# Performance work log

Hardware: AMD Instinct MI355X
Metric: run time of the kernel (lower is better)

The kernel has to match this reference:

```python
import jax, jax.numpy as jnp
import numpy as np

EPS = 1e-8  # torch CosineSimilarity eps


def setup_inputs() -> dict:
    key = jax.random.key(0)
    ks = jax.random.split(key, 7)
    B, N, T, C, M, MEM, IN, E = 8, 512, 64, 128, 32, 20, 2, 4
    s = 0.05  # keep softmax logits in a sane range (xavier-like scale)
    return {
        "input": jax.random.normal(ks[0], (B, N, T, IN), jnp.float32),
        "hidden": jax.random.normal(ks[1], (E, B, N, T, C), jnp.float32),
        "memory": jax.random.normal(ks[2], (MEM, M), jnp.float32) * s,
        "input_query": jax.random.normal(ks[3], (IN, M), jnp.float32) * s,
        "Wq": jax.random.normal(ks[4], (E, C, M), jnp.float32) * s,
        "Wk": jax.random.normal(ks[5], (E, C, M), jnp.float32) * s,
        "Wv": jax.random.normal(ks[6], (E, C, M), jnp.float32) * s,
    }


def _cosine_sim(a, b):
    # torch.nn.CosineSimilarity(dim=-1): dot / (max(||a||,eps)*max(||b||,eps))
    num = jnp.sum(a * b, axis=-1)
    na = jnp.maximum(jnp.linalg.norm(a, axis=-1), EPS)
    nb = jnp.maximum(jnp.linalg.norm(b, axis=-1), EPS)
    return num / (na * nb)


def reference(input, hidden, memory, input_query, Wq, Wk, Wv):
    B, N, T, _ = input.shape
    out_dim = 1
    # query_mem: soft read from memory bank -> [B,N,T,mem_hid]
    q_in = jnp.einsum("bnti,im->bntm", input, input_query)
    mem_score = jax.nn.softmax(jnp.einsum("bntm,km->bntk", q_in, memory), axis=-1)
    memories = jnp.einsum("bntk,km->bntm", mem_score, memory)
    # per-expert self-attention over T (vectorized over the 4 experts)
    q = jnp.einsum("ebntc,ecm->ebntm", hidden, Wq)
    k = jnp.einsum("ebntc,ecm->ebntm", hidden, Wk)
    v = jnp.einsum("ebntc,ecm->ebntm", hidden, Wv)
    energy = jnp.einsum("ebntm,ebnsm->ebnts", q, k)  # [E,B,N,T,T]
    att = jnp.einsum("ebnts,ebnsm->ebntm", jax.nn.softmax(energy, axis=-1), v)
    # cosine similarity of memory read vs each expert's attended hidden
    scores = _cosine_sim(memories[None], att)  # [E,B,N,T]
    scores = jnp.moveaxis(scores, 0, -1)  # [B,N,T,E]
    out = jnp.broadcast_to(scores[..., None, :], (B, N, T, out_dim, scores.shape[-1]))
    return out
```

## Files before the change

kernel.cpp:

```cpp
#include <hip/hip_runtime.h>
#include <hip/hip_bf16.h>
#include <math.h>

#define Bc 8
#define Nc 512
#define Tc 64
#define Cc 128
#define Mc 32
#define MEMc 20
#define Ec 4

#define LDK  40
#define LDVT 72

typedef short bf16x8 __attribute__((ext_vector_type(8)));
typedef float f32x4  __attribute__((ext_vector_type(4)));

__device__ __forceinline__ unsigned short f2bfu(float f) {
    return __builtin_bit_cast(unsigned short, __float2bfloat16(f));
}
__device__ __forceinline__ unsigned pk2bf(float x, float y) {
    return ((unsigned)f2bfu(y) << 16) | (unsigned)f2bfu(x);
}

__device__ __forceinline__ void gload_lds16(const void* g, void* l) {
    __builtin_amdgcn_global_load_lds(
        (const __attribute__((address_space(1))) unsigned int*)g,
        (__attribute__((address_space(3))) unsigned int*)l, 16, 0, 0);
}

__global__ void prep(const float* __restrict__ Wq, const float* __restrict__ Wk,
                     const float* __restrict__ Wv, const float* __restrict__ membank,
                     const float* __restrict__ iq,
                     short* __restrict__ wt_img, short* __restrict__ bankM,
                     float* __restrict__ G2) {
    const int t = threadIdx.x;
    if (blockIdx.x < 192) {
        int idx = blockIdx.x * 256 + t;
        int e   = idx / 12288;
        int r   = idx - e * 12288;
        int mat = r >> 12;
        int m   = (r >> 7) & 31;
        int c   = r & 127;
        const float* W = (mat == 0) ? Wq : (mat == 1) ? Wk : Wv;
        const int dst = e * 12288 + mat * 4096 + m * 128 + (c ^ ((m & 7) << 3));
        wt_img[dst] = (short)f2bfu(W[((size_t)e * Cc + c) * Mc + m]);
    } else {
        for (int idx = t; idx < Mc * 32; idx += 256) {
            int m = idx >> 5, k = idx & 31;
            bankM[idx] = (short)f2bfu((k < MEMc) ? membank[k * Mc + m] : 0.f);
        }
        if (t < MEMc) {
            float g0 = 0.f, g1 = 0.f;
            for (int m = 0; m < Mc; ++m) {
                float b = membank[t * Mc + m];
                g0 = fmaf(iq[m], b, g0);
                g1 = fmaf(iq[Mc + m], b, g1);
            }
            G2[2 * t]     = g0;
            G2[2 * t + 1] = g1;
        }
    }
}

__device__ __forceinline__ void proj(const short* __restrict__ sh_wt, const bf16x8* a,
                                     int lo, int hi,
                                     f32x4 q_[2], f32x4 k_[2], f32x4 v_[2]) {
    #pragma unroll
    for (int nt = 0; nt < 2; ++nt)
        q_[nt] = k_[nt] = v_[nt] = (f32x4){0.f, 0.f, 0.f, 0.f};
    const int swz = (lo & 7) << 3;
    int col[4];
    #pragma unroll
    for (int kt = 0; kt < 4; ++kt) col[kt] = (kt * 32 + hi * 8) ^ swz;
    const short* wrow = sh_wt + lo * 128;
    #pragma unroll
    for (int nt = 0; nt < 2; ++nt) {
        const short* p0 = wrow + nt * 2048;
        #pragma unroll
        for (int kt = 0; kt < 4; ++kt) {
            const bf16x8 wq = *(const bf16x8*)(p0 + col[kt]);
            const bf16x8 wk = *(const bf16x8*)(p0 + 4096 + col[kt]);
            const bf16x8 wv = *(const bf16x8*)(p0 + 8192 + col[kt]);
            q_[nt] = __builtin_amdgcn_mfma_f32_16x16x32_bf16(wq, a[kt], q_[nt], 0, 0, 0);
            k_[nt] = __builtin_amdgcn_mfma_f32_16x16x32_bf16(wk, a[kt], k_[nt], 0, 0, 0);
            v_[nt] = __builtin_amdgcn_mfma_f32_16x16x32_bf16(wv, a[kt], v_[nt], 0, 0, 0);
        }
    }
}

__device__ __forceinline__ void gate_pd(const float* __restrict__ G2, float2 in2, unsigned pd[10]) {
    #pragma unroll
    for (int kp = 0; kp < 10; ++kp) {
        const float4 g = *(const float4*)(G2 + 4 * kp);
        pd[kp] = pk2bf(__expf(in2.x * g.x + in2.y * g.y),
                       __expf(in2.x * g.z + in2.y * g.w));
    }
}

__device__ __forceinline__ void mem_read(const short* __restrict__ bankM,
                                         const unsigned pd[10], int lo, int hi, int w,
                                         f32x4 am[2]) {
    am[0] = am[1] = (f32x4){0.f, 0.f, 0.f, 0.f};
    const int addrD = (w * 16 + lo) * 4;
    unsigned Wd[10];
    #pragma unroll
    for (int u = 0; u < 10; ++u)
        Wd[u] = __builtin_amdgcn_ds_bpermute(addrD, (int)pd[u]);
    unsigned b[4];
    #pragma unroll
    for (int u = 0; u < 4; ++u) {
        const unsigned l_ = (hi == 0) ? Wd[u] : Wd[4 + u];
        const unsigned h_ = (u < 2) ? ((hi == 2) ? Wd[8 + u] : 0u) : 0u;
        b[u] = (hi < 2) ? l_ : h_;
    }
    const bf16x8 bp2 = __builtin_bit_cast(bf16x8, (uint4){b[0], b[1], b[2], b[3]});
    #pragma unroll
    for (int nt = 0; nt < 2; ++nt) {
        const bf16x8 ab = *(const bf16x8*)(bankM + (nt * 16 + lo) * 32 + hi * 8);
        am[nt] = __builtin_amdgcn_mfma_f32_16x16x32_bf16(ab, bp2, am[nt], 0, 0, 0);
    }
}

__device__ __forceinline__ void attend_store(
    const short* __restrict__ shk, const short* __restrict__ shv,
    const unsigned q_pk[4], const f32x4 am[2],
    int lo, int hi, int w, int A01, int A23, int addrA, int addrB,
    int bn, int e, float* __restrict__ out) {
    unsigned pw[4][2];
    {
        unsigned l0 = __builtin_amdgcn_ds_bpermute(A01, (int)q_pk[0]);
        unsigned h0_ = __builtin_amdgcn_ds_bpermute(A01, (int)q_pk[2]);
        unsigned l1 = __builtin_amdgcn_ds_bpermute(A01, (int)q_pk[1]);
        unsigned h1_ = __builtin_amdgcn_ds_bpermute(A01, (int)q_pk[3]);
        unsigned l2 = __builtin_amdgcn_ds_bpermute(A23, (int)q_pk[0]);
        unsigned h2_ = __builtin_amdgcn_ds_bpermute(A23, (int)q_pk[2]);
        unsigned l3 = __builtin_amdgcn_ds_bpermute(A23, (int)q_pk[1]);
        unsigned h3_ = __builtin_amdgcn_ds_bpermute(A23, (int)q_pk[3]);
        const bf16x8 bq = __builtin_bit_cast(bf16x8, (uint4){
            (hi < 2) ? l0 : h0_, (hi < 2) ? l1 : h1_,
            (hi < 2) ? l2 : h2_, (hi < 2) ? l3 : h3_});
        #pragma unroll
        for (int st = 0; st < 4; ++st) {
            const bf16x8 akf = *(const bf16x8*)&shk[(st * 16 + lo) * LDK + hi * 8];
            const f32x4 en = __builtin_amdgcn_mfma_f32_16x16x32_bf16(
                akf, bq, (f32x4){0.f, 0.f, 0.f, 0.f}, 0, 0, 0);
            pw[st][0] = pk2bf(__expf(en[0]), __expf(en[1]));
            pw[st][1] = pk2bf(__expf(en[2]), __expf(en[3]));
        }
    }
    f32x4 av[2];
    av[0] = av[1] = (f32x4){0.f, 0.f, 0.f, 0.f};
    {
        bf16x8 bp[2];
        #pragma unroll
        for (int kt = 0; kt < 2; ++kt) {
            unsigned wrd[4];
            #pragma unroll
            for (int uu = 0; uu < 4; ++uu) {
                const int adr = (uu < 2) ? addrA : addrB;
                const unsigned ev = __builtin_amdgcn_ds_bpermute(adr, (int)pw[2 * kt][uu & 1]);
                const unsigned od = __builtin_amdgcn_ds_bpermute(adr, (int)pw[2 * kt + 1][uu & 1]);
                wrd[uu] = (hi < 2) ? ev : od;
            }
            bp[kt] = __builtin_bit_cast(bf16x8, (uint4){wrd[0], wrd[1], wrd[2], wrd[3]});
        }
        #pragma unroll
        for (int nt = 0; nt < 2; ++nt)
            #pragma unroll
            for (int kt = 0; kt < 2; ++kt) {
                const bf16x8 avt = *(const bf16x8*)&shv[(nt * 16 + lo) * LDVT + kt * 32 + hi * 8];
                av[nt] = __builtin_amdgcn_mfma_f32_16x16x32_bf16(avt, bp[kt], av[nt], 0, 0, 0);
            }
    }
    float d = 0.f, na = 0.f, nb = 0.f;
    #pragma unroll
    for (int nt = 0; nt < 2; ++nt)
        #pragma unroll
        for (int j = 0; j < 4; ++j) {
            const float av_ = av[nt][j], am_ = am[nt][j];
            d  = fmaf(av_, am_, d);
            na = fmaf(av_, av_, na);
            nb = fmaf(am_, am_, nb);
        }
    d  += __shfl_xor(d, 16);  d  += __shfl_xor(d, 32);
    na += __shfl_xor(na, 16); na += __shfl_xor(na, 32);
    nb += __shfl_xor(nb, 16); nb += __shfl_xor(nb, 32);
    if (hi == 0) {
        const float denom = fmaxf(sqrtf(na), 1e-8f) * fmaxf(sqrtf(nb), 1e-8f);
        out[((size_t)bn * Tc + w * 16 + lo) * Ec + e] = d / denom;
    }
}

__global__ __launch_bounds__(256, 4) void mg_mfma(
    const float* __restrict__ input,
    const float* __restrict__ hidden,
    const short* __restrict__ wt_img,
    const short* __restrict__ bankM,
    const float* __restrict__ G2,
    float* __restrict__ out)
{
    __shared__ __align__(16) short sh_wt[12288];
    __shared__ __align__(16) short sh_k [Tc * LDK];
    __shared__ __align__(16) short sh_vt[Mc * LDVT];

    const int t    = threadIdx.x;
    const int w    = t >> 6;
    const int lane = t & 63;
    const int lo   = lane & 15;
    const int hi   = lane >> 4;
    const int e    = blockIdx.x >> 11;
    const int bn0  = (blockIdx.x & 2047) * 2;
    const int bn1  = bn0 + 1;

    const int A01   = (((hi & 1) * 32) + lo) << 2;
    const int A23   = A01 + 64;
    const int addrA = (((hi & 1) * 2 + 0) * 16 + lo) * 4;
    const int addrB = (((hi & 1) * 2 + 1) * 16 + lo) * 4;

    {
        const short* gsrc = wt_img + (size_t)e * 12288 + w * 512 + lane * 8;
        short* ldst = sh_wt + w * 512;
        #pragma unroll
        for (int c = 0; c < 6; ++c)
            gload_lds16(gsrc + c * 2048, ldst + c * 2048);
    }

    const float2 in2_0 = *(const float2*)(input + ((size_t)bn0 * Tc + lane) * 2);
    const float2 in2_1 = *(const float2*)(input + ((size_t)bn1 * Tc + lane) * 2);
    float4 h[8];
    {
        const float* hr0 = hidden + (((size_t)(e * 4096 + bn0)) * Tc + w * 16 + lo) * Cc + hi * 8;
        #pragma unroll
        for (int kt = 0; kt < 4; ++kt) {
            h[2 * kt]     = *(const float4*)(hr0 + kt * 32);
            h[2 * kt + 1] = *(const float4*)(hr0 + kt * 32 + 4);
        }
    }

    f32x4 am0[2];
    {
        unsigned pd0[10];
        gate_pd(G2, in2_0, pd0);
        mem_read(bankM, pd0, lo, hi, w, am0);
    }

    bf16x8 a0[4];
    #pragma unroll
    for (int kt = 0; kt < 4; ++kt) {
        const float4 x = h[2 * kt], y = h[2 * kt + 1];
        a0[kt] = __builtin_bit_cast(bf16x8, (uint4){pk2bf(x.x, x.y), pk2bf(x.z, x.w),
                                                    pk2bf(y.x, y.y), pk2bf(y.z, y.w)});
    }

    __syncthreads();

    unsigned q_pk0[4];
    {
        f32x4 q_[2], k_[2], v_[2];
        proj(sh_wt, a0, lo, hi, q_, k_, v_);
        #pragma unroll
        for (int nt = 0; nt < 2; ++nt) {
            *(uint2*)&sh_k[(w * 16 + lo) * LDK + nt * 16 + hi * 4] =
                (uint2){pk2bf(k_[nt][0], k_[nt][1]), pk2bf(k_[nt][2], k_[nt][3])};
            #pragma unroll
            for (int j = 0; j < 4; ++j)
                sh_vt[(nt * 16 + hi * 4 + j) * LDVT + w * 16 + lo] = (short)f2bfu(v_[nt][j]);
            q_pk0[nt * 2]     = pk2bf(q_[nt][0], q_[nt][1]);
            q_pk0[nt * 2 + 1] = pk2bf(q_[nt][2], q_[nt][3]);
        }
    }

    __syncthreads();

    {
        const float* hr1 = hidden + (((size_t)(e * 4096 + bn1)) * Tc + w * 16 + lo) * Cc + hi * 8;
        #pragma unroll
        for (int kt = 0; kt < 4; ++kt) {
            h[2 * kt]     = *(const float4*)(hr1 + kt * 32);
            h[2 * kt + 1] = *(const float4*)(hr1 + kt * 32 + 4);
        }
    }

    f32x4 am1[2];
    {
        unsigned pd1[10];
        gate_pd(G2, in2_1, pd1);
        mem_read(bankM, pd1, lo, hi, w, am1);
    }

    attend_store(sh_k, sh_vt, q_pk0, am0, lo, hi, w, A01, A23, addrA, addrB, bn0, e, out);

    bf16x8 a1[4];
    #pragma unroll
    for (int kt = 0; kt < 4; ++kt) {
        const float4 x = h[2 * kt], y = h[2 * kt + 1];
        a1[kt] = __builtin_bit_cast(bf16x8, (uint4){pk2bf(x.x, x.y), pk2bf(x.z, x.w),
                                                    pk2bf(y.x, y.y), pk2bf(y.z, y.w)});
    }

    __syncthreads();

    unsigned q_pk1[4];
    {
        f32x4 q_[2], k_[2], v_[2];
        proj(sh_wt, a1, lo, hi, q_, k_, v_);
        #pragma unroll
        for (int nt = 0; nt < 2; ++nt) {
            *(uint2*)&sh_k[(w * 16 + lo) * LDK + nt * 16 + hi * 4] =
                (uint2){pk2bf(k_[nt][0], k_[nt][1]), pk2bf(k_[nt][2], k_[nt][3])};
            #pragma unroll
            for (int j = 0; j < 4; ++j)
                sh_vt[(nt * 16 + hi * 4 + j) * LDVT + w * 16 + lo] = (short)f2bfu(v_[nt][j]);
            q_pk1[nt * 2]     = pk2bf(q_[nt][0], q_[nt][1]);
            q_pk1[nt * 2 + 1] = pk2bf(q_[nt][2], q_[nt][3]);
        }
    }

    __syncthreads();

    attend_store(sh_k, sh_vt, q_pk1, am1, lo, hi, w, A01, A23, addrA, addrB, bn1, e, out);
}

extern "C" void kernel_launch(void* const* d_in, const int* in_sizes, int n_in,
                              void* d_out, int out_size, void* d_ws, size_t ws_size,
                              hipStream_t stream) {
    const float* input   = (const float*)d_in[0];
    const float* hidden  = (const float*)d_in[1];
    const float* membank = (const float*)d_in[2];
    const float* iq      = (const float*)d_in[3];
    const float* Wq      = (const float*)d_in[4];
    const float* Wk      = (const float*)d_in[5];
    const float* Wv      = (const float*)d_in[6];
    float* out = (float*)d_out;

    short* wt_img = (short*)d_ws;
    short* bankM  = (short*)((char*)d_ws + 98304);
    float* G2     = (float*)((char*)d_ws + 100352);

    prep<<<193, 256, 0, stream>>>(Wq, Wk, Wv, membank, iq, wt_img, bankM, G2);
    mg_mfma<<<Ec * Bc * Nc / 2, 256, 0, stream>>>(input, hidden, wt_img, bankM, G2, out);
}
```

Measured before the change: 121.4 us.

## Process eight (b,n) units per block with software-pipelined hidden loads

Each block now handles eight consecutive (b,n) units instead of two, so the weight image is staged into LDS once per eight units rather than once per two. The per-unit phase prefetches the next unit's hidden rows before doing the memory read and attention for the current unit, overlapping global loads with compute. The cost is four times fewer blocks (2048), which reduces parallelism and tail balance, plus more live registers from the eight preloaded input pairs.

```diff
diff --git a/kernel.cpp b/kernel.cpp
--- a/kernel.cpp
+++ b/kernel.cpp
@@ -12,6 +12,8 @@
 
 #define LDK  40
 #define LDVT 72
+
+#define UNITS 8
 
 typedef short bf16x8 __attribute__((ext_vector_type(8)));
 typedef float f32x4  __attribute__((ext_vector_type(4)));
@@ -63,9 +65,27 @@
     }
 }
 
-__device__ __forceinline__ void proj(const short* __restrict__ sh_wt, const bf16x8* a,
-                                     int lo, int hi,
-                                     f32x4 q_[2], f32x4 k_[2], f32x4 v_[2]) {
+__device__ __forceinline__ void load_hidden(const float* __restrict__ hrow, float4 h[8]) {
+    #pragma unroll
+    for (int kt = 0; kt < 4; ++kt) {
+        h[2 * kt]     = *(const float4*)(hrow + kt * 32);
+        h[2 * kt + 1] = *(const float4*)(hrow + kt * 32 + 4);
+    }
+}
+__device__ __forceinline__ void conv_a(const float4 h[8], bf16x8 a[4]) {
+    #pragma unroll
+    for (int kt = 0; kt < 4; ++kt) {
+        const float4 x = h[2 * kt], y = h[2 * kt + 1];
+        a[kt] = __builtin_bit_cast(bf16x8, (uint4){pk2bf(x.x, x.y), pk2bf(x.z, x.w),
+                                                   pk2bf(y.x, y.y), pk2bf(y.z, y.w)});
+    }
+}
+
+__device__ __forceinline__ void proj_store(const short* __restrict__ sh_wt, const bf16x8 a[4],
+                                           int lo, int hi, int w,
+                                           short* __restrict__ sh_k, short* __restrict__ sh_vt,
+                                           unsigned q_pk[4]) {
+    f32x4 q_[2], k_[2], v_[2];
     #pragma unroll
     for (int nt = 0; nt < 2; ++nt)
         q_[nt] = k_[nt] = v_[nt] = (f32x4){0.f, 0.f, 0.f, 0.f};
@@ -86,6 +106,16 @@
             k_[nt] = __builtin_amdgcn_mfma_f32_16x16x32_bf16(wk, a[kt], k_[nt], 0, 0, 0);
             v_[nt] = __builtin_amdgcn_mfma_f32_16x16x32_bf16(wv, a[kt], v_[nt], 0, 0, 0);
         }
+    }
+    #pragma unroll
+    for (int nt = 0; nt < 2; ++nt) {
+        *(uint2*)&sh_k[(w * 16 + lo) * LDK + nt * 16 + hi * 4] =
+            (uint2){pk2bf(k_[nt][0], k_[nt][1]), pk2bf(k_[nt][2], k_[nt][3])};
+        #pragma unroll
+        for (int j = 0; j < 4; ++j)
+            sh_vt[(nt * 16 + hi * 4 + j) * LDVT + w * 16 + lo] = (short)f2bfu(v_[nt][j]);
+        q_pk[nt * 2]     = pk2bf(q_[nt][0], q_[nt][1]);
+        q_pk[nt * 2 + 1] = pk2bf(q_[nt][2], q_[nt][3]);
     }
 }
 
@@ -209,9 +239,8 @@
     const int lane = t & 63;
     const int lo   = lane & 15;
     const int hi   = lane >> 4;
-    const int e    = blockIdx.x >> 11;
-    const int bn0  = (blockIdx.x & 2047) * 2;
-    const int bn1  = bn0 + 1;
+    const int e    = blockIdx.x >> 9;
+    const int bnb  = (blockIdx.x & 511) * UNITS;
 
     const int A01   = (((hi & 1) * 32) + lo) << 2;
     const int A23   = A01 + 64;
@@ -226,100 +255,48 @@
             gload_lds16(gsrc + c * 2048, ldst + c * 2048);
     }
 
-    const float2 in2_0 = *(const float2*)(input + ((size_t)bn0 * Tc + lane) * 2);
-    const float2 in2_1 = *(const float2*)(input + ((size_t)bn1 * Tc + lane) * 2);
-    float4 h[8];
-    {
-        const float* hr0 = hidden + (((size_t)(e * 4096 + bn0)) * Tc + w * 16 + lo) * Cc + hi * 8;
-        #pragma unroll
-        for (int kt = 0; kt < 4; ++kt) {
-            h[2 * kt]     = *(const float4*)(hr0 + kt * 32);
-            h[2 * kt + 1] = *(const float4*)(hr0 + kt * 32 + 4);
-        }
-    }
-
-    f32x4 am0[2];
-    {
-        unsigned pd0[10];
-        gate_pd(G2, in2_0, pd0);
-        mem_read(bankM, pd0, lo, hi, w, am0);
-    }
-
-    bf16x8 a0[4];
-    #pragma unroll
-    for (int kt = 0; kt < 4; ++kt) {
-        const float4 x = h[2 * kt], y = h[2 * kt + 1];
-        a0[kt] = __builtin_bit_cast(bf16x8, (uint4){pk2bf(x.x, x.y), pk2bf(x.z, x.w),
-                                                    pk2bf(y.x, y.y), pk2bf(y.z, y.w)});
-    }
-
+    float2 in2[UNITS];
+    #pragma unroll
+    for (int u = 0; u < UNITS; ++u)
+        in2[u] = *(const float2*)(input + ((size_t)(bnb + u) * Tc + lane) * 2);
+
+    const float* hbase = hidden + (((size_t)(e * 4096 + bnb)) * Tc + w * 16 + lo) * Cc + hi * 8;
+
+    float4  h[8];
+    bf16x8  a[4];
+    unsigned q_pk[4];
+
+    load_hidden(hbase, h);
+    conv_a(h, a);
     __syncthreads();
-
-    unsigned q_pk0[4];
-    {
-        f32x4 q_[2], k_[2], v_[2];
-        proj(sh_wt, a0, lo, hi, q_, k_, v_);
-        #pragma unroll
-        for (int nt = 0; nt < 2; ++nt) {
-            *(uint2*)&sh_k[(w * 16 + lo) * LDK + nt * 16 + hi * 4] =
-                (uint2){pk2bf(k_[nt][0], k_[nt][1]), pk2bf(k_[nt][2], k_[nt][3])};
-            #pragma unroll
-            for (int j = 0; j < 4; ++j)
-                sh_vt[(nt * 16 + hi * 4 + j) * LDVT + w * 16 + lo] = (short)f2bfu(v_[nt][j]);
-            q_pk0[nt * 2]     = pk2bf(q_[nt][0], q_[nt][1]);
-            q_pk0[nt * 2 + 1] = pk2bf(q_[nt][2], q_[nt][3]);
-        }
-    }
-
+    proj_store(sh_wt, a, lo, hi, w, sh_k, sh_vt, q_pk);
     __syncthreads();
 
-    {
-        const float* hr1 = hidden + (((size_t)(e * 4096 + bn1)) * Tc + w * 16 + lo) * Cc + hi * 8;
-        #pragma unroll
-        for (int kt = 0; kt < 4; ++kt) {
-            h[2 * kt]     = *(const float4*)(hr1 + kt * 32);
-            h[2 * kt + 1] = *(const float4*)(hr1 + kt * 32 + 4);
-        }
-    }
-
-    f32x4 am1[2];
-    {
-        unsigned pd1[10];
-        gate_pd(G2, in2_1, pd1);
-        mem_read(bankM, pd1, lo, hi, w, am1);
-    }
-
-    attend_store(sh_k, sh_vt, q_pk0, am0, lo, hi, w, A01, A23, addrA, addrB, bn0, e, out);
-
-    bf16x8 a1[4];
-    #pragma unroll
-    for (int kt = 0; kt < 4; ++kt) {
-        const float4 x = h[2 * kt], y = h[2 * kt + 1];
-        a1[kt] = __builtin_bit_cast(bf16x8, (uint4){pk2bf(x.x, x.y), pk2bf(x.z, x.w),
-                                                    pk2bf(y.x, y.y), pk2bf(y.z, y.w)});
-    }
-
-    __syncthreads();
-
-    unsigned q_pk1[4];
-    {
-        f32x4 q_[2], k_[2], v_[2];
-        proj(sh_wt, a1, lo, hi, q_, k_, v_);
-        #pragma unroll
-        for (int nt = 0; nt < 2; ++nt) {
-            *(uint2*)&sh_k[(w * 16 + lo) * LDK + nt * 16 + hi * 4] =
-                (uint2){pk2bf(k_[nt][0], k_[nt][1]), pk2bf(k_[nt][2], k_[nt][3])};
-            #pragma unroll
-            for (int j = 0; j < 4; ++j)
-                sh_vt[(nt * 16 + hi * 4 + j) * LDVT + w * 16 + lo] = (short)f2bfu(v_[nt][j]);
-            q_pk1[nt * 2]     = pk2bf(q_[nt][0], q_[nt][1]);
-            q_pk1[nt * 2 + 1] = pk2bf(q_[nt][2], q_[nt][3]);
-        }
-    }
-
-    __syncthreads();
-
-    attend_store(sh_k, sh_vt, q_pk1, am1, lo, hi, w, A01, A23, addrA, addrB, bn1, e, out);
+#define PHASE(U, NOT_LAST) do {                                                   \
+        if (NOT_LAST) load_hidden(hbase + (U + 1) * (Tc * Cc), h);                \
+        unsigned pd[10];                                                          \
+        gate_pd(G2, in2[U], pd);                                                  \
+        f32x4 am[2];                                                              \
+        mem_read(bankM, pd, lo, hi, w, am);                                       \
+        attend_store(sh_k, sh_vt, q_pk, am, lo, hi, w, A01, A23, addrA, addrB,    \
+                     bnb + U, e, out);                                            \
+        if (NOT_LAST) {                                                           \
+            conv_a(h, a);                                                         \
+            __syncthreads();              \
+            proj_store(sh_wt, a, lo, hi, w, sh_k, sh_vt, q_pk);                   \
+            __syncthreads();                                  \
+        }                                                                         \
+    } while (0)
+
+    PHASE(0, 1);
+    PHASE(1, 1);
+    PHASE(2, 1);
+    PHASE(3, 1);
+    PHASE(4, 1);
+    PHASE(5, 1);
+    PHASE(6, 1);
+    PHASE(7, 0);
+#undef PHASE
 }
 
 extern "C" void kernel_launch(void* const* d_in, const int* in_sizes, int n_in,
@@ -339,5 +316,5 @@
     float* G2     = (float*)((char*)d_ws + 100352);
 
     prep<<<193, 256, 0, stream>>>(Wq, Wk, Wv, membank, iq, wt_img, bankM, G2);
-    mg_mfma<<<Ec * Bc * Nc / 2, 256, 0, stream>>>(input, hidden, wt_img, bankM, G2, out);
-}
+    mg_mfma<<<Ec * Bc * Nc / UNITS, 256, 0, stream>>>(input, hidden, wt_img, bankM, G2, out);
+}
```

Result: slower. 127.8 us (+5.2%).
